# Kernel optimization log

Hardware: AMD Instinct MI355X
Metric: run time of the kernel (lower is better)

## Reference

```python
import jax, jax.numpy as jnp
import numpy as np
from jax import lax
import math

C = 512
B = 8
T = 8192


def _kaiser_sinc_filter1d(cutoff, half_width, kernel_size):
    # exact port of torch kaiser_sinc_filter1d (even kernel branch for k=12)
    half_size = kernel_size // 2
    delta_f = 4.0 * half_width
    A = 2.285 * (half_size - 1) * math.pi * delta_f + 7.95
    if A > 50.0:
        beta = 0.1102 * (A - 8.7)
    elif A >= 21.0:
        beta = 0.5842 * (A - 21.0) ** 0.4 + 0.07886 * (A - 21.0)
    else:
        beta = 0.0
    window = np.kaiser(kernel_size, beta)  # symmetric == torch periodic=False
    if kernel_size % 2 == 0:
        time = np.arange(-half_size, half_size) + 0.5
    else:
        time = np.arange(kernel_size) - half_size
    filt = 2.0 * cutoff * window * np.sinc(2.0 * cutoff * time)
    filt = filt / filt.sum()
    return filt.astype(np.float32)  # [kernel_size]


def _make_up_down_filters(channels, ratio=2, kernel_size=12):
    f = _kaiser_sinc_filter1d(0.5 / ratio, 0.5 / ratio, kernel_size)
    # upsample weight: polyphase split of f*ratio -> [2,1,6], repeat per channel -> [2C,1,6]
    w = f * ratio
    p0, p1 = w[0::2], w[1::2]
    up = np.stack([p0, p1], axis=0)[:, None, :]            # [2,1,6]
    up = np.tile(up, (channels, 1, 1))                     # [2C,1,6]
    # downsample (low-pass) weight: [C,1,12]
    down = np.tile(f.reshape(1, 1, kernel_size), (channels, 1, 1))
    return jnp.asarray(up), jnp.asarray(down)


def _conv1d(x, w, stride=1, padding=0, dilation=1, groups=1):
    return lax.conv_general_dilated(
        x, w, window_strides=(stride,), padding=[(padding, padding)],
        rhs_dilation=(dilation,), dimension_numbers=('NCH', 'OIH', 'NCH'),
        feature_group_count=groups)


def _snake_beta(x, alpha, beta):
    # alpha_logscale=True
    a = jnp.exp(alpha)[None, :, None]
    b = jnp.exp(beta)[None, :, None]
    return x + (1.0 - jnp.cos(2.0 * a * x)) / (2.0 * b + 1e-9)


def _upsample(x, up_filt):
    b, c, _ = x.shape
    xp = jnp.pad(x, ((0, 0), (0, 0), (2, 3)))
    out = _conv1d(xp, up_filt, groups=c)                   # [B, 2C, T']
    out = out.reshape(b, c, 2, -1)                         # (channel, phase) split
    out = jnp.transpose(out, (0, 1, 3, 2)).reshape(b, c, -1)  # interleave phases
    return out[..., 2:-2]                                  # [B, C, 2T-4]


def _downsample(x, down_filt):
    c = x.shape[1]
    return _conv1d(x, down_filt, stride=2, padding=5, groups=c)


def _activation1d(x, alpha, beta, up_filt, down_filt):
    x = _upsample(x, up_filt)
    x = _snake_beta(x, alpha, beta)
    return _downsample(x, down_filt)


def _wn_weight(v, g):
    # weight_norm (dim=0): w = g * v / ||v||, norm over (in, k) per output channel
    norm = jnp.sqrt(jnp.sum(v * v, axis=(1, 2), keepdims=True))
    return g[:, None, None] * v / norm


def setup_inputs() -> dict:
    key = jax.random.key(0)
    ks = jax.random.split(key, 12)
    x = jax.random.normal(ks[0], (B, C, T), dtype=jnp.float32)
    alpha1 = 0.1 * jax.random.normal(ks[1], (C,), dtype=jnp.float32)
    beta1 = 0.1 * jax.random.normal(ks[2], (C,), dtype=jnp.float32)
    alpha2 = 0.1 * jax.random.normal(ks[3], (C,), dtype=jnp.float32)
    beta2 = 0.1 * jax.random.normal(ks[4], (C,), dtype=jnp.float32)
    scale = 1.0 / np.sqrt(C * 3)
    v1 = scale * jax.random.normal(ks[5], (C, C, 3), dtype=jnp.float32)
    g1 = jax.random.uniform(ks[6], (C,), dtype=jnp.float32, minval=0.5, maxval=1.5)
    b1 = 0.01 * jax.random.normal(ks[7], (C,), dtype=jnp.float32)
    v2 = scale * jax.random.normal(ks[8], (C, C, 3), dtype=jnp.float32)
    g2 = jax.random.uniform(ks[9], (C,), dtype=jnp.float32, minval=0.5, maxval=1.5)
    b2 = 0.01 * jax.random.normal(ks[10], (C,), dtype=jnp.float32)
    up_filt, down_filt = _make_up_down_filters(C)
    return dict(x=x, alpha1=alpha1, beta1=beta1, alpha2=alpha2, beta2=beta2,
                v1=v1, g1=g1, b1=b1, v2=v2, g2=g2, b2=b2,
                up_filt=up_filt, down_filt=down_filt)


def reference(x, alpha1, beta1, alpha2, beta2, v1, g1, b1, v2, g2, b2,
              up_filt, down_filt):
    w1 = _wn_weight(v1, g1)
    w2 = _wn_weight(v2, g2)
    # dilation = (1,3,5) -> convs1 uses dilation[0] = 1, padding = get_padding(3,1) = 1
    xt = _activation1d(x, alpha1, beta1, up_filt, down_filt)    # [B,C,T-2]
    xt = _conv1d(xt, w1, padding=1, dilation=1) + b1[None, :, None]
    xt = _activation1d(xt, alpha2, beta2, up_filt, down_filt)   # [B,C,T-4]
    xt = _conv1d(xt, w2, padding=1, dilation=1) + b2[None, :, None]
    x_residual = x[..., :xt.shape[2]]                            # narrow(2, 0, T-4)
    return xt + x_residual
```

## Files before the change

### kernel.cpp

```cpp
#include <hip/hip_runtime.h>
#include <hip/hip_bf16.h>

#define CCH 512
#define BATCH 8
#define TLEN 8192
#define RPITCH ((size_t)TLEN * CCH)

using f32x4 = __attribute__((ext_vector_type(4))) float;
using s16x8 = __attribute__((ext_vector_type(8))) short;
using s16x4 = __attribute__((ext_vector_type(4))) short;

__device__ __forceinline__ float b2f(short s) {
    union { unsigned int i; float f; } u; u.i = ((unsigned int)(unsigned short)s) << 16; return u.f;
}
__device__ __forceinline__ short f2b(float f) {
    __hip_bfloat16 h = __float2bfloat16(f);
    return *reinterpret_cast<short*>(&h);
}

__device__ __forceinline__ void glds16(const void* g, void* l) {
    __builtin_amdgcn_global_load_lds(
        (const __attribute__((address_space(1))) unsigned int*)g,
        (__attribute__((address_space(3))) unsigned int*)l, 16, 0, 0);
}

__global__ __launch_bounds__(256) void wn_pack_kernel(const float* __restrict__ v,
                                                      const float* __restrict__ g,
                                                      short* __restrict__ wp)
{
    int co = blockIdx.x;
    const float* vr = v + (size_t)co * (CCH * 3);
    float s = 0.f;
    for (int i = threadIdx.x; i < CCH * 3; i += 256) { float xv = vr[i]; s += xv * xv; }
#pragma unroll
    for (int off = 32; off > 0; off >>= 1) s += __shfl_down(s, off);
    __shared__ float red[4];
    int lane = threadIdx.x & 63, wv = threadIdx.x >> 6;
    if (lane == 0) red[wv] = s;
    __syncthreads();
    float tot = red[0] + red[1] + red[2] + red[3];
    float scale = g[co] / sqrtf(tot);
    for (int i = threadIdx.x; i < CCH * 3; i += 256) {
        int ci = i / 3, tap = i - ci * 3;
        size_t dst = ((size_t)(((ci >> 5) * 4 + (co >> 7)) * 3 + tap)) * 4096
                     + (size_t)(co & 127) * 32 + (ci & 31);
        wp[dst] = f2b(vr[i] * scale);
    }
}

__global__ __launch_bounds__(256) void transpose_kernel(const float* __restrict__ x,
                                                        short* __restrict__ out)
{
    __shared__ float ls[64][65];
    int tid = threadIdx.x;
    int t0 = blockIdx.x * 64, c0 = blockIdx.y * 64, b = blockIdx.z;
    const float* xb = x + (size_t)b * CCH * TLEN;
#pragma unroll
    for (int p = 0; p < 4; ++p) {
        int c = p * 16 + (tid >> 4);
        int t4 = (tid & 15) * 4;
        f32x4 v = *(const f32x4*)&xb[(size_t)(c0 + c) * TLEN + t0 + t4];
#pragma unroll
        for (int i = 0; i < 4; ++i) ls[c][t4 + i] = v[i];
    }
    __syncthreads();
    short* ob = out + (size_t)b * RPITCH;
#pragma unroll
    for (int p = 0; p < 16; ++p) {
        int idx = p * 256 + tid;
        int t = idx >> 6, c = idx & 63;
        ob[(size_t)(t0 + t) * CCH + c0 + c] = f2b(ls[c][t]);
    }
}

#define ALT 256
__global__ __launch_bounds__(256) void act_kernel(
    const short* __restrict__ in, short* __restrict__ out,
    const float* __restrict__ alpha, const float* __restrict__ beta,
    const float* __restrict__ upf, const float* __restrict__ dwf,
    int Tin, int Tout)
{
    int tid = threadIdx.x;
    int c = blockIdx.y * 256 + tid;
    int b = blockIdx.z;
    int t0 = blockIdx.x * ALT;
    const short* ib = in + (size_t)b * RPITCH;
    short* ob = out + (size_t)b * RPITCH;

    float ph0[6], ph1[6], fw[12];
#pragma unroll
    for (int m = 0; m < 6; ++m) { ph0[m] = upf[m]; ph1[m] = upf[6 + m]; }
#pragma unroll
    for (int k = 0; k < 12; ++k) fw[k] = dwf[k];

    float a     = __expf(alpha[c]);
    float inv2b = 1.f / (2.f * __expf(beta[c]) + 1e-9f);
    float twoa  = 2.f * a;
    int Ls = 2 * Tin - 4;

    auto ldx = [&](int t) -> float {
        return (t >= 0 && t < Tin) ? b2f(ib[(size_t)t * CCH + c]) : 0.f;
    };
    auto snake = [&](float u) -> float {
        return u + (1.f - __cosf(twoa * u)) * inv2b;
    };

    float xa[12];
#pragma unroll
    for (int i = 0; i < 12; ++i) xa[i] = ldx(t0 - 4 + i);
    float sr[12];
#pragma unroll
    for (int i = 0; i < 12; ++i) {
        int j = 2 * t0 - 5 + i;
        int xoff = ((i - 3) >> 1) + 2;
        const float* ph = ((i + 1) & 1) ? ph1 : ph0;
        float u = 0.f;
#pragma unroll
        for (int m = 0; m < 6; ++m) u += ph[m] * xa[xoff + m];
        sr[i] = (j >= 0 && j < Ls) ? snake(u) : 0.f;
    }
    float xw[7];
#pragma unroll
    for (int m = 0; m < 6; ++m) xw[m] = xa[6 + m];
    xw[6] = ldx(t0 + 8);

#pragma unroll 4
    for (int it = 0; it < ALT; ++it) {
        int t = t0 + it;
        float y = 0.f;
#pragma unroll
        for (int k = 0; k < 12; ++k) y += fw[k] * sr[k];
        if (t < Tout) ob[(size_t)t * CCH + c] = f2b(y);
        float u1 = 0.f, u2 = 0.f;
#pragma unroll
        for (int m = 0; m < 6; ++m) { u1 += ph1[m] * xw[m]; u2 += ph0[m] * xw[m + 1]; }
        float s1 = (2 * t + 7 < Ls) ? snake(u1) : 0.f;
        float s2 = (2 * t + 8 < Ls) ? snake(u2) : 0.f;
#pragma unroll
        for (int i = 0; i < 10; ++i) sr[i] = sr[i + 2];
        sr[10] = s1; sr[11] = s2;
#pragma unroll
        for (int m = 0; m < 6; ++m) xw[m] = xw[m + 1];
        xw[6] = ldx(t + 9);
    }
}

template <int MODE>
__global__ __launch_bounds__(256) void conv_mfma(
    const short* __restrict__ xin, const short* __restrict__ wp,
    const float* __restrict__ bias, const float* __restrict__ resid,
    float* __restrict__ outF, short* __restrict__ outT, int rows)
{
    __shared__ __align__(16) short wlds[3 * 128 * 32];
    __shared__ __align__(16) short ilds[132 * 32];
    int tid = threadIdx.x;
    int wave = tid >> 6, lane = tid & 63;
    int quad = lane >> 4, l16 = lane & 15;
    int wm = wave >> 1, wn = wave & 1;
    int t0 = blockIdx.x * 128, cog = blockIdx.y, b = blockIdx.z;

    const short* inb = xin + (size_t)b * RPITCH;
    f32x4 acc[4][4];
#pragma unroll
    for (int i = 0; i < 4; ++i)
#pragma unroll
        for (int j = 0; j < 4; ++j) acc[i][j] = 0.f;

    bool interior = (t0 >= 1) && (t0 + 129 <= rows);

    for (int cc = 0; cc < 16; ++cc) {
        const short* wsrc = wp + (size_t)(cc * 4 + cog) * (3 * 128 * 32);
#pragma unroll
        for (int p = 0; p < 6; ++p) {
            int seg = wave * 6 + p;
            glds16(wsrc + seg * 512 + lane * 8, wlds + seg * 512);
        }
        const short* isrc = inb + (size_t)(t0 - 1) * CCH + cc * 32;
        if (interior) {
#pragma unroll
            for (int p = 0; p < 2; ++p) {
                int seg0 = (p * 4 + wave) * 64;
                int s = seg0 + lane;
                glds16(isrc + (size_t)(s >> 2) * CCH + (s & 3) * 8, ilds + seg0 * 8);
            }
            if (wave == 0 && lane < 8) {
                int s = 512 + lane;
                glds16(isrc + (size_t)(s >> 2) * CCH + (s & 3) * 8, ilds + 512 * 8);
            }
        } else {
            for (int s = tid; s < 520; s += 256) {
                int gt = t0 - 1 + (s >> 2);
                s16x8 v = 0;
                if (gt >= 0 && gt < rows)
                    v = *(const s16x8*)(inb + (size_t)gt * CCH + cc * 32 + (s & 3) * 8);
                *(s16x8*)(ilds + s * 8) = v;
            }
        }
        __syncthreads();
#pragma unroll
        for (int tap = 0; tap < 3; ++tap) {
            s16x8 af[4], bv[4];
#pragma unroll
            for (int mf = 0; mf < 4; ++mf)
                af[mf] = *(const s16x8*)(wlds + tap * 4096 + (wm * 64 + mf * 16 + l16) * 32 + quad * 8);
#pragma unroll
            for (int nf = 0; nf < 4; ++nf)
                bv[nf] = *(const s16x8*)(ilds + (wn * 64 + nf * 16 + l16 + tap) * 32 + quad * 8);
#pragma unroll
            for (int mf = 0; mf < 4; ++mf)
#pragma unroll
                for (int nf = 0; nf < 4; ++nf)
                    acc[mf][nf] = __builtin_amdgcn_mfma_f32_16x16x32_bf16(
                        af[mf], bv[nf], acc[mf][nf], 0, 0, 0);
        }
        __syncthreads();
    }

    f32x4 b4[4];
#pragma unroll
    for (int mf = 0; mf < 4; ++mf)
        b4[mf] = *(const f32x4*)(bias + cog * 128 + wm * 64 + mf * 16 + quad * 4);

#pragma unroll
    for (int mf = 0; mf < 4; ++mf) {
#pragma unroll
        for (int nf = 0; nf < 4; ++nf) {
            int t = t0 + wn * 64 + nf * 16 + l16;
            if (t >= rows) continue;
            if (MODE == 0) {
                int co = cog * 128 + wm * 64 + mf * 16 + quad * 4;
                s16x4 o;
#pragma unroll
                for (int r = 0; r < 4; ++r) o[r] = f2b(acc[mf][nf][r] + b4[mf][r]);
                *(s16x4*)(outT + (size_t)b * RPITCH + (size_t)t * CCH + co) = o;
            } else {
#pragma unroll
                for (int r = 0; r < 4; ++r) {
                    int co = cog * 128 + wm * 64 + mf * 16 + quad * 4 + r;
                    size_t rb = (size_t)b * CCH + co;
                    outF[rb * (size_t)rows + t] =
                        acc[mf][nf][r] + b4[mf][r] + resid[rb * (size_t)TLEN + t];
                }
            }
        }
    }
}

extern "C" void kernel_launch(void* const* d_in, const int* in_sizes, int n_in,
                              void* d_out, int out_size, void* d_ws, size_t ws_size,
                              hipStream_t stream)
{
    const float* x      = (const float*)d_in[0];
    const float* alpha1 = (const float*)d_in[1];
    const float* beta1  = (const float*)d_in[2];
    const float* alpha2 = (const float*)d_in[3];
    const float* beta2  = (const float*)d_in[4];
    const float* v1     = (const float*)d_in[5];
    const float* g1     = (const float*)d_in[6];
    const float* b1     = (const float*)d_in[7];
    const float* v2     = (const float*)d_in[8];
    const float* g2     = (const float*)d_in[9];
    const float* b2     = (const float*)d_in[10];
    const float* upf    = (const float*)d_in[11];
    const float* dwf    = (const float*)d_in[12];
    float* out = (float*)d_out;

    const int T1 = TLEN - 2;
    const int T2 = TLEN - 4;

    char* wsb = (char*)d_ws;
    short* w1p = (short*)wsb;
    short* w2p = w1p + (size_t)CCH * CCH * 3;
    short* bufX = w2p + (size_t)CCH * CCH * 3;
    short* bufY = bufX + (size_t)BATCH * RPITCH;

    wn_pack_kernel<<<CCH, 256, 0, stream>>>(v1, g1, w1p);
    wn_pack_kernel<<<CCH, 256, 0, stream>>>(v2, g2, w2p);

    transpose_kernel<<<dim3(TLEN / 64, CCH / 64, BATCH), 256, 0, stream>>>(x, bufX);

    act_kernel<<<dim3((T1 + ALT - 1) / ALT, CCH / 256, BATCH), 256, 0, stream>>>(
        bufX, bufY, alpha1, beta1, upf, dwf, TLEN, T1);

    conv_mfma<0><<<dim3((T1 + 127) / 128, 4, BATCH), 256, 0, stream>>>(
        bufY, w1p, b1, nullptr, nullptr, bufX, T1);

    act_kernel<<<dim3((T2 + ALT - 1) / ALT, CCH / 256, BATCH), 256, 0, stream>>>(
        bufX, bufY, alpha2, beta2, upf, dwf, T1, T2);

    conv_mfma<1><<<dim3((T2 + 127) / 128, 4, BATCH), 256, 0, stream>>>(
        bufY, w2p, b2, x, out, nullptr, T2);
}
```

Measured before the change: 767.0 us.

## Double-buffer conv LDS staging, stage coalesced epilogues, vectorize activation and transpose stores

The conv kernel now double-buffers weight and input tiles in LDS, so the next channel chunk's async global-to-LDS loads are issued while the current chunk's MFMAs run. Both epilogues go through LDS so stores are wide and coalesced, with the residual add using float4 loads. The activation kernel handles two adjacent channels per thread with paired bf16 loads and stores and a smaller time tile. The transpose writes 4-wide vectors, and the conv grid is flattened so the four output-channel groups of a time tile are adjacent. The costs are doubled LDS per block, which may lower occupancy, and extra barriers in the epilogue.

```diff
diff --git a/kernel.cpp b/kernel.cpp
--- a/kernel.cpp
+++ b/kernel.cpp
@@ -9,6 +9,7 @@
 using f32x4 = __attribute__((ext_vector_type(4))) float;
 using s16x8 = __attribute__((ext_vector_type(8))) short;
 using s16x4 = __attribute__((ext_vector_type(4))) short;
+using s16x2 = __attribute__((ext_vector_type(2))) short;
 
 __device__ __forceinline__ float b2f(short s) {
     union { unsigned int i; float f; } u; u.i = ((unsigned int)(unsigned short)s) << 16; return u.f;
@@ -66,14 +67,62 @@
     __syncthreads();
     short* ob = out + (size_t)b * RPITCH;
 #pragma unroll
-    for (int p = 0; p < 16; ++p) {
-        int idx = p * 256 + tid;
-        int t = idx >> 6, c = idx & 63;
-        ob[(size_t)(t0 + t) * CCH + c0 + c] = f2b(ls[c][t]);
-    }
-}
-
-#define ALT 256
+    for (int p = 0; p < 4; ++p) {
+        int t = p * 16 + (tid >> 4);
+        int c4 = (tid & 15) * 4;
+        s16x4 o;
+#pragma unroll
+        for (int i = 0; i < 4; ++i) o[i] = f2b(ls[c4 + i][t]);
+        *(s16x4*)(ob + (size_t)(t0 + t) * CCH + c0 + c4) = o;
+#pragma unroll
+        for (int q = 1; q < 4; ++q) {
+            int t2 = p * 16 + (tid >> 4) + q * 0;
+        }
+    }
+#pragma unroll
+    for (int p = 4; p < 16; ++p) {
+        int t = (p - 4) * 16 + 16 + (tid >> 4) + ((p - 4) / 3) * 0;
+        (void)t;
+        break;
+    }
+#pragma unroll
+    for (int p = 0; p < 4; ++p) {
+        int base_t = p * 16 + (tid >> 4);
+        int c4 = (tid & 15) * 4;
+        (void)base_t; (void)c4;
+    }
+    __syncthreads();
+}
+
+__global__ __launch_bounds__(256) void transpose_kernel2(const float* __restrict__ x,
+                                                         short* __restrict__ out)
+{
+    __shared__ float ls[64][65];
+    int tid = threadIdx.x;
+    int t0 = blockIdx.x * 64, c0 = blockIdx.y * 64, b = blockIdx.z;
+    const float* xb = x + (size_t)b * CCH * TLEN;
+#pragma unroll
+    for (int p = 0; p < 4; ++p) {
+        int c = p * 16 + (tid >> 4);
+        int t4 = (tid & 15) * 4;
+        f32x4 v = *(const f32x4*)&xb[(size_t)(c0 + c) * TLEN + t0 + t4];
+#pragma unroll
+        for (int i = 0; i < 4; ++i) ls[c][t4 + i] = v[i];
+    }
+    __syncthreads();
+    short* ob = out + (size_t)b * RPITCH;
+#pragma unroll
+    for (int p = 0; p < 4; ++p) {
+        int t = p * 16 + (tid >> 4);
+        int c4 = (tid & 15) * 4;
+        s16x4 o;
+#pragma unroll
+        for (int i = 0; i < 4; ++i) o[i] = f2b(ls[c4 + i][t]);
+        *(s16x4*)(ob + (size_t)(t0 + t) * CCH + c0 + c4) = o;
+    }
+}
+
+#define ALT 128
 __global__ __launch_bounds__(256) void act_kernel(
     const short* __restrict__ in, short* __restrict__ out,
     const float* __restrict__ alpha, const float* __restrict__ beta,
@@ -81,11 +130,11 @@
     int Tin, int Tout)
 {
     int tid = threadIdx.x;
-    int c = blockIdx.y * 256 + tid;
+    int c2 = tid * 2;
     int b = blockIdx.z;
     int t0 = blockIdx.x * ALT;
-    const short* ib = in + (size_t)b * RPITCH;
-    short* ob = out + (size_t)b * RPITCH;
+    const short* ib = in + (size_t)b * RPITCH + c2;
+    short* ob = out + (size_t)b * RPITCH + c2;
 
     float ph0[6], ph1[6], fw[12];
 #pragma unroll
@@ -93,55 +142,77 @@
 #pragma unroll
     for (int k = 0; k < 12; ++k) fw[k] = dwf[k];
 
-    float a     = __expf(alpha[c]);
-    float inv2b = 1.f / (2.f * __expf(beta[c]) + 1e-9f);
-    float twoa  = 2.f * a;
+    float twoa[2], inv2b[2];
+#pragma unroll
+    for (int ch = 0; ch < 2; ++ch) {
+        twoa[ch]  = 2.f * __expf(alpha[c2 + ch]);
+        inv2b[ch] = 1.f / (2.f * __expf(beta[c2 + ch]) + 1e-9f);
+    }
     int Ls = 2 * Tin - 4;
 
-    auto ldx = [&](int t) -> float {
-        return (t >= 0 && t < Tin) ? b2f(ib[(size_t)t * CCH + c]) : 0.f;
+    auto ldx2 = [&](int t, float* dst) {
+        if (t >= 0 && t < Tin) {
+            s16x2 v = *(const s16x2*)(ib + (size_t)t * CCH);
+            dst[0] = b2f(v[0]); dst[1] = b2f(v[1]);
+        } else { dst[0] = 0.f; dst[1] = 0.f; }
     };
-    auto snake = [&](float u) -> float {
-        return u + (1.f - __cosf(twoa * u)) * inv2b;
-    };
-
-    float xa[12];
-#pragma unroll
-    for (int i = 0; i < 12; ++i) xa[i] = ldx(t0 - 4 + i);
-    float sr[12];
+
+    float xa[12][2];
+#pragma unroll
+    for (int i = 0; i < 12; ++i) ldx2(t0 - 4 + i, xa[i]);
+    float sr[12][2];
 #pragma unroll
     for (int i = 0; i < 12; ++i) {
         int j = 2 * t0 - 5 + i;
         int xoff = ((i - 3) >> 1) + 2;
         const float* ph = ((i + 1) & 1) ? ph1 : ph0;
-        float u = 0.f;
-#pragma unroll
-        for (int m = 0; m < 6; ++m) u += ph[m] * xa[xoff + m];
-        sr[i] = (j >= 0 && j < Ls) ? snake(u) : 0.f;
-    }
-    float xw[7];
-#pragma unroll
-    for (int m = 0; m < 6; ++m) xw[m] = xa[6 + m];
-    xw[6] = ldx(t0 + 8);
+        bool ok = (j >= 0 && j < Ls);
+#pragma unroll
+        for (int ch = 0; ch < 2; ++ch) {
+            float u = 0.f;
+#pragma unroll
+            for (int m = 0; m < 6; ++m) u += ph[m] * xa[xoff + m][ch];
+            sr[i][ch] = ok ? (u + (1.f - __cosf(twoa[ch] * u)) * inv2b[ch]) : 0.f;
+        }
+    }
+    float xw[7][2];
+#pragma unroll
+    for (int m = 0; m < 6; ++m) { xw[m][0] = xa[6 + m][0]; xw[m][1] = xa[6 + m][1]; }
+    ldx2(t0 + 8, xw[6]);
 
 #pragma unroll 4
     for (int it = 0; it < ALT; ++it) {
         int t = t0 + it;
-        float y = 0.f;
-#pragma unroll
-        for (int k = 0; k < 12; ++k) y += fw[k] * sr[k];
-        if (t < Tout) ob[(size_t)t * CCH + c] = f2b(y);
-        float u1 = 0.f, u2 = 0.f;
-#pragma unroll
-        for (int m = 0; m < 6; ++m) { u1 += ph1[m] * xw[m]; u2 += ph0[m] * xw[m + 1]; }
-        float s1 = (2 * t + 7 < Ls) ? snake(u1) : 0.f;
-        float s2 = (2 * t + 8 < Ls) ? snake(u2) : 0.f;
-#pragma unroll
-        for (int i = 0; i < 10; ++i) sr[i] = sr[i + 2];
-        sr[10] = s1; sr[11] = s2;
-#pragma unroll
-        for (int m = 0; m < 6; ++m) xw[m] = xw[m + 1];
-        xw[6] = ldx(t + 9);
+        float y[2] = {0.f, 0.f};
+#pragma unroll
+        for (int k = 0; k < 12; ++k) {
+            y[0] += fw[k] * sr[k][0];
+            y[1] += fw[k] * sr[k][1];
+        }
+        if (t < Tout) {
+            s16x2 o; o[0] = f2b(y[0]); o[1] = f2b(y[1]);
+            *(s16x2*)(ob + (size_t)t * CCH) = o;
+        }
+        bool ok1 = (2 * t + 7 < Ls), ok2 = (2 * t + 8 < Ls);
+        float s1[2], s2[2];
+#pragma unroll
+        for (int ch = 0; ch < 2; ++ch) {
+            float u1 = 0.f, u2 = 0.f;
+#pragma unroll
+            for (int m = 0; m < 6; ++m) {
+                u1 += ph1[m] * xw[m][ch];
+                u2 += ph0[m] * xw[m + 1][ch];
+            }
+            s1[ch] = ok1 ? (u1 + (1.f - __cosf(twoa[ch] * u1)) * inv2b[ch]) : 0.f;
+            s2[ch] = ok2 ? (u2 + (1.f - __cosf(twoa[ch] * u2)) * inv2b[ch]) : 0.f;
+        }
+#pragma unroll
+        for (int i = 0; i < 10; ++i) { sr[i][0] = sr[i + 2][0]; sr[i][1] = sr[i + 2][1]; }
+        sr[10][0] = s1[0]; sr[10][1] = s1[1];
+        sr[11][0] = s2[0]; sr[11][1] = s2[1];
+#pragma unroll
+        for (int m = 0; m < 6; ++m) { xw[m][0] = xw[m + 1][0]; xw[m][1] = xw[m + 1][1]; }
+        ldx2(t + 9, xw[6]);
     }
 }
 
@@ -151,29 +222,30 @@
     const float* __restrict__ bias, const float* __restrict__ resid,
     float* __restrict__ outF, short* __restrict__ outT, int rows)
 {
-    __shared__ __align__(16) short wlds[3 * 128 * 32];
-    __shared__ __align__(16) short ilds[132 * 32];
+    constexpr int WB = 3 * 128 * 32;
+    constexpr int IB = 132 * 32;
+    __shared__ __align__(16) short lds[2 * (WB + IB)];
+
     int tid = threadIdx.x;
     int wave = tid >> 6, lane = tid & 63;
     int quad = lane >> 4, l16 = lane & 15;
     int wm = wave >> 1, wn = wave & 1;
-    int t0 = blockIdx.x * 128, cog = blockIdx.y, b = blockIdx.z;
+    int bx = blockIdx.x;
+    int cog = bx & 3, tt = bx >> 2;
+    int t0 = tt * 128, b = blockIdx.z;
 
     const short* inb = xin + (size_t)b * RPITCH;
-    f32x4 acc[4][4];
-#pragma unroll
-    for (int i = 0; i < 4; ++i)
-#pragma unroll
-        for (int j = 0; j < 4; ++j) acc[i][j] = 0.f;
-
     bool interior = (t0 >= 1) && (t0 + 129 <= rows);
 
-    for (int cc = 0; cc < 16; ++cc) {
-        const short* wsrc = wp + (size_t)(cc * 4 + cog) * (3 * 128 * 32);
+    auto stage = [&](int cc, int pb) {
+        short* base = lds + pb * (WB + IB);
+        short* wl = base;
+        short* il = base + WB;
+        const short* wsrc = wp + (size_t)(cc * 4 + cog) * WB;
 #pragma unroll
         for (int p = 0; p < 6; ++p) {
             int seg = wave * 6 + p;
-            glds16(wsrc + seg * 512 + lane * 8, wlds + seg * 512);
+            glds16(wsrc + seg * 512 + lane * 8, wl + seg * 512);
         }
         const short* isrc = inb + (size_t)(t0 - 1) * CCH + cc * 32;
         if (interior) {
@@ -181,11 +253,11 @@
             for (int p = 0; p < 2; ++p) {
                 int seg0 = (p * 4 + wave) * 64;
                 int s = seg0 + lane;
-                glds16(isrc + (size_t)(s >> 2) * CCH + (s & 3) * 8, ilds + seg0 * 8);
+                glds16(isrc + (size_t)(s >> 2) * CCH + (s & 3) * 8, il + seg0 * 8);
             }
             if (wave == 0 && lane < 8) {
                 int s = 512 + lane;
-                glds16(isrc + (size_t)(s >> 2) * CCH + (s & 3) * 8, ilds + 512 * 8);
+                glds16(isrc + (size_t)(s >> 2) * CCH + (s & 3) * 8, il + 512 * 8);
             }
         } else {
             for (int s = tid; s < 520; s += 256) {
@@ -193,19 +265,35 @@
                 s16x8 v = 0;
                 if (gt >= 0 && gt < rows)
                     v = *(const s16x8*)(inb + (size_t)gt * CCH + cc * 32 + (s & 3) * 8);
-                *(s16x8*)(ilds + s * 8) = v;
-            }
-        }
-        __syncthreads();
+                *(s16x8*)(il + s * 8) = v;
+            }
+        }
+    };
+
+    f32x4 acc[4][4];
+#pragma unroll
+    for (int i = 0; i < 4; ++i)
+#pragma unroll
+        for (int j = 0; j < 4; ++j) acc[i][j] = 0.f;
+
+    stage(0, 0);
+    __syncthreads();
+
+    for (int cc = 0; cc < 16; ++cc) {
+        int pb = cc & 1;
+        if (cc < 15) stage(cc + 1, pb ^ 1);
+        const short* base = lds + pb * (WB + IB);
+        const short* wl = base;
+        const short* il = base + WB;
 #pragma unroll
         for (int tap = 0; tap < 3; ++tap) {
             s16x8 af[4], bv[4];
 #pragma unroll
             for (int mf = 0; mf < 4; ++mf)
-                af[mf] = *(const s16x8*)(wlds + tap * 4096 + (wm * 64 + mf * 16 + l16) * 32 + quad * 8);
+                af[mf] = *(const s16x8*)(wl + tap * 4096 + (wm * 64 + mf * 16 + l16) * 32 + quad * 8);
 #pragma unroll
             for (int nf = 0; nf < 4; ++nf)
-                bv[nf] = *(const s16x8*)(ilds + (wn * 64 + nf * 16 + l16 + tap) * 32 + quad * 8);
+                bv[nf] = *(const s16x8*)(il + (wn * 64 + nf * 16 + l16 + tap) * 32 + quad * 8);
 #pragma unroll
             for (int mf = 0; mf < 4; ++mf)
 #pragma unroll
@@ -221,27 +309,68 @@
     for (int mf = 0; mf < 4; ++mf)
         b4[mf] = *(const f32x4*)(bias + cog * 128 + wm * 64 + mf * 16 + quad * 4);
 
-#pragma unroll
-    for (int mf = 0; mf < 4; ++mf) {
-#pragma unroll
-        for (int nf = 0; nf < 4; ++nf) {
-            int t = t0 + wn * 64 + nf * 16 + l16;
-            if (t >= rows) continue;
-            if (MODE == 0) {
-                int co = cog * 128 + wm * 64 + mf * 16 + quad * 4;
+    if (MODE == 0) {
+        short* ot = lds;
+#pragma unroll
+        for (int mf = 0; mf < 4; ++mf)
+#pragma unroll
+            for (int nf = 0; nf < 4; ++nf) {
+                int t = wn * 64 + nf * 16 + l16;
+                int co = wm * 64 + mf * 16 + quad * 4;
                 s16x4 o;
 #pragma unroll
                 for (int r = 0; r < 4; ++r) o[r] = f2b(acc[mf][nf][r] + b4[mf][r]);
-                *(s16x4*)(outT + (size_t)b * RPITCH + (size_t)t * CCH + co) = o;
-            } else {
-#pragma unroll
-                for (int r = 0; r < 4; ++r) {
-                    int co = cog * 128 + wm * 64 + mf * 16 + quad * 4 + r;
-                    size_t rb = (size_t)b * CCH + co;
-                    outF[rb * (size_t)rows + t] =
-                        acc[mf][nf][r] + b4[mf][r] + resid[rb * (size_t)TLEN + t];
+                *(s16x4*)(ot + t * 136 + co) = o;
+            }
+        __syncthreads();
+#pragma unroll
+        for (int rr = 0; rr < 8; ++rr) {
+            int idx = rr * 256 + tid;
+            int tr = idx >> 4, c8 = (idx & 15) * 8;
+            int t = t0 + tr;
+            if (t < rows)
+                *(s16x8*)(outT + (size_t)b * RPITCH + (size_t)t * CCH + cog * 128 + c8)
+                    = *(const s16x8*)(ot + tr * 136 + c8);
+        }
+    } else {
+        float* of = (float*)lds;
+#pragma unroll
+        for (int h = 0; h < 2; ++h) {
+            if (wm == h) {
+#pragma unroll
+                for (int mf = 0; mf < 4; ++mf)
+#pragma unroll
+                    for (int nf = 0; nf < 4; ++nf) {
+                        int t = wn * 64 + nf * 16 + l16;
+#pragma unroll
+                        for (int r = 0; r < 4; ++r)
+                            of[(mf * 16 + quad * 4 + r) * 132 + t] = acc[mf][nf][r] + b4[mf][r];
+                    }
+            }
+            __syncthreads();
+#pragma unroll
+            for (int rr = 0; rr < 8; ++rr) {
+                int idx = rr * 256 + tid;
+                int row = idx >> 5, c4 = (idx & 31) * 4;
+                int co = cog * 128 + h * 64 + row;
+                int t = t0 + c4;
+                f32x4 v = *(const f32x4*)(of + row * 132 + c4);
+                size_t ro = (size_t)b * CCH + co;
+                const float* rrow = resid + ro * TLEN;
+                float* orow = outF + ro * (size_t)rows;
+                if (t + 3 < rows) {
+                    f32x4 rv = *(const f32x4*)(rrow + t);
+                    f32x4 ov;
+#pragma unroll
+                    for (int i = 0; i < 4; ++i) ov[i] = v[i] + rv[i];
+                    *(f32x4*)(orow + t) = ov;
+                } else {
+#pragma unroll
+                    for (int i = 0; i < 4; ++i)
+                        if (t + i < rows) orow[t + i] = v[i] + rrow[t + i];
                 }
             }
+            __syncthreads();
         }
     }
 }
@@ -277,17 +406,17 @@
     wn_pack_kernel<<<CCH, 256, 0, stream>>>(v1, g1, w1p);
     wn_pack_kernel<<<CCH, 256, 0, stream>>>(v2, g2, w2p);
 
-    transpose_kernel<<<dim3(TLEN / 64, CCH / 64, BATCH), 256, 0, stream>>>(x, bufX);
-
-    act_kernel<<<dim3((T1 + ALT - 1) / ALT, CCH / 256, BATCH), 256, 0, stream>>>(
+    transpose_kernel2<<<dim3(TLEN / 64, CCH / 64, BATCH), 256, 0, stream>>>(x, bufX);
+
+    act_kernel<<<dim3((TLEN + ALT - 1) / ALT, 1, BATCH), 256, 0, stream>>>(
         bufX, bufY, alpha1, beta1, upf, dwf, TLEN, T1);
 
-    conv_mfma<0><<<dim3((T1 + 127) / 128, 4, BATCH), 256, 0, stream>>>(
+    conv_mfma<0><<<dim3(256, 1, BATCH), 256, 0, stream>>>(
         bufY, w1p, b1, nullptr, nullptr, bufX, T1);
 
-    act_kernel<<<dim3((T2 + ALT - 1) / ALT, CCH / 256, BATCH), 256, 0, stream>>>(
+    act_kernel<<<dim3((T1 + ALT - 1) / ALT, 1, BATCH), 256, 0, stream>>>(
         bufX, bufY, alpha2, beta2, upf, dwf, T1, T2);
 
-    conv_mfma<1><<<dim3((T2 + 127) / 128, 4, BATCH), 256, 0, stream>>>(
+    conv_mfma<1><<<dim3(256, 1, BATCH), 256, 0, stream>>>(
         bufY, w2p, b2, x, out, nullptr, T2);
 }
```

Result: faster. 678.4 us (-11.5%).
